# Optimization experiments

Measured on AMD Instinct MI355X. Metric: run time of the kernel, lower is better.

The kernel has to match this reference:

```python
import jax, jax.numpy as jnp
import numpy as np
import math

D_MODEL = 1024
NUM_HEADS = 16
BATCH = 2
SEQ = 2048

def setup_inputs() -> dict:
    key = jax.random.key(0)
    ks = jax.random.split(key, 9)
    s = 1.0 / math.sqrt(D_MODEL)
    inp = {
        "X": jax.random.normal(ks[0], (BATCH, SEQ, D_MODEL), dtype=jnp.float32),
        "Wq": jax.random.uniform(ks[1], (D_MODEL, D_MODEL), jnp.float32, -s, s),
        "bq": jax.random.uniform(ks[2], (D_MODEL,), jnp.float32, -s, s),
        "Wk": jax.random.uniform(ks[3], (D_MODEL, D_MODEL), jnp.float32, -s, s),
        "bk": jax.random.uniform(ks[4], (D_MODEL,), jnp.float32, -s, s),
        "Wv": jax.random.uniform(ks[5], (D_MODEL, D_MODEL), jnp.float32, -s, s),
        "bv": jax.random.uniform(ks[6], (D_MODEL,), jnp.float32, -s, s),
        "Wo": jax.random.uniform(ks[7], (D_MODEL, D_MODEL), jnp.float32, -s, s),
        "bo": jax.random.uniform(ks[8], (D_MODEL,), jnp.float32, -s, s),
    }
    return inp

def reference(X, Wq, bq, Wk, bk, Wv, bv, Wo, bo):
    B, S, D = X.shape
    H = NUM_HEADS
    dk = D // H
    # QKV projections (Linear: x @ W.T + b; here W stored as [in, out] so x @ W + b)
    q = X @ Wq + bq
    k = X @ Wk + bk
    v = X @ Wv + bv
    # split heads -> [B, H, S, dk]
    q = q.reshape(B, S, H, dk).transpose(0, 2, 1, 3)
    k = k.reshape(B, S, H, dk).transpose(0, 2, 1, 3)
    v = v.reshape(B, S, H, dk).transpose(0, 2, 1, 3)
    scores = jnp.einsum("bhqd,bhkd->bhqk", q, k) / math.sqrt(dk)
    weights = jax.nn.softmax(scores, axis=-1)
    attn = jnp.einsum("bhqk,bhkd->bhqd", weights, v)
    concat = attn.transpose(0, 2, 1, 3).reshape(B, S, D)
    return concat @ Wo + bo
```

## Files before the change

### kernel.cpp

```cpp
#include <hip/hip_runtime.h>
#include <stdint.h>

#define D_MODEL 1024
#define NH      16
#define DKH     64
#define BATCH   2
#define SEQ     2048
#define M_TOK   (BATCH*SEQ)

typedef __attribute__((ext_vector_type(8))) short bf16x8;
typedef __attribute__((ext_vector_type(4))) float f32x4;

__device__ __forceinline__ uint16_t f2b(float f) {
  uint32_t u = __builtin_bit_cast(uint32_t, f);
  return (uint16_t)((u + 0x7FFFu + ((u >> 16) & 1u)) >> 16);
}

__device__ __forceinline__ void gl2lds16(const uint16_t* g, uint16_t* l) {
  __builtin_amdgcn_global_load_lds(
      (const __attribute__((address_space(1))) void*)g,
      (__attribute__((address_space(3))) void*)l, 16, 0, 0);
}

__global__ __launch_bounds__(256) void prep(
    const float* __restrict__ X, uint16_t* __restrict__ Xb,
    const float* __restrict__ W0, const float* __restrict__ W1,
    const float* __restrict__ W2, const float* __restrict__ W3,
    uint16_t* __restrict__ T0, uint16_t* __restrict__ T1,
    uint16_t* __restrict__ T2, uint16_t* __restrict__ T3) {
  const int bid = blockIdx.x;
  if (bid < 2048) {
    int i = (bid * 256 + threadIdx.x) * 8;
    float4 a = *(const float4*)(X + i);
    float4 b = *(const float4*)(X + i + 4);
    uint16_t tmp[8] = {f2b(a.x), f2b(a.y), f2b(a.z), f2b(a.w),
                       f2b(b.x), f2b(b.y), f2b(b.z), f2b(b.w)};
    *(uint4*)(Xb + i) = *(const uint4*)tmp;
  } else {
    __shared__ float tile[32][33];
    int r = bid - 2048;
    int z = r >> 10, tt = r & 1023;
    const float* W = (z == 0) ? W0 : (z == 1) ? W1 : (z == 2) ? W2 : W3;
    uint16_t*    T = (z == 0) ? T0 : (z == 1) ? T1 : (z == 2) ? T2 : T3;
    int k0 = (tt & 31) * 32, n0 = (tt >> 5) * 32;
    int t = threadIdx.x;
    int rr = t >> 3, c4 = (t & 7) * 4;
    float4 v = *(const float4*)(W + (size_t)(k0 + rr) * D_MODEL + n0 + c4);
    tile[rr][c4] = v.x; tile[rr][c4 + 1] = v.y;
    tile[rr][c4 + 2] = v.z; tile[rr][c4 + 3] = v.w;
    __syncthreads();
    uint16_t o[4] = {f2b(tile[c4][rr]), f2b(tile[c4 + 1][rr]),
                     f2b(tile[c4 + 2][rr]), f2b(tile[c4 + 3][rr])};
    *(uint2*)(T + (size_t)(n0 + rr) * D_MODEL + k0 + c4) = *(const uint2*)o;
  }
}

template <bool SWAP>
__device__ __forceinline__ void gemm_core(const uint16_t* __restrict__ A,
                                          const uint16_t* __restrict__ BT,
                                          uint16_t* As, uint16_t* Bs,
                                          int m0, int n0, int kBeg, int kEnd,
                                          f32x4 (&acc)[4][4]) {
  const int t    = threadIdx.x;
  const int lane = t & 63;
  const int qi   = lane & 15, g = lane >> 4;
  const int wm   = (t >> 7) & 1;
  const int wn   = (t >> 6) & 1;
  const int srow = t >> 2;
  const int sc   = (t & 3) ^ ((t >> 3) & 3);
  const int wbase = t & 192;
  const int rch  = (g ^ ((qi >> 1) & 3)) * 8;

  const uint16_t* Ag = A  + (size_t)(m0 + srow) * D_MODEL + sc * 8;
  const uint16_t* Bg = BT + (size_t)(n0 + srow) * D_MODEL + sc * 8;

#pragma unroll
  for (int j = 0; j < 2; j++) {
    gl2lds16(Ag + (size_t)j * 64 * D_MODEL + kBeg, As + (j * 256 + wbase) * 8);
    gl2lds16(Bg + (size_t)j * 64 * D_MODEL + kBeg, Bs + (j * 256 + wbase) * 8);
  }

  int cur = 0;
  for (int k0 = kBeg; k0 < kEnd; k0 += 32) {
    __syncthreads();
    int kn = k0 + 32;
    if (kn < kEnd) {
      int nb = (cur ^ 1) * 4096;
#pragma unroll
      for (int j = 0; j < 2; j++) {
        gl2lds16(Ag + (size_t)j * 64 * D_MODEL + kn, As + nb + (j * 256 + wbase) * 8);
        gl2lds16(Bg + (size_t)j * 64 * D_MODEL + kn, Bs + nb + (j * 256 + wbase) * 8);
      }
    }
    const uint16_t* Ab = As + cur * 4096;
    const uint16_t* Bb = Bs + cur * 4096;
    bf16x8 af[4], bf[4];
#pragma unroll
    for (int i = 0; i < 4; i++) {
      af[i] = *(const bf16x8*)(Ab + (wm * 64 + i * 16 + qi) * 32 + rch);
      bf[i] = *(const bf16x8*)(Bb + (wn * 64 + i * 16 + qi) * 32 + rch);
    }
#pragma unroll
    for (int i = 0; i < 4; i++)
#pragma unroll
      for (int j = 0; j < 4; j++)
        acc[i][j] = SWAP
          ? __builtin_amdgcn_mfma_f32_16x16x32_bf16(bf[j], af[i], acc[i][j], 0, 0, 0)
          : __builtin_amdgcn_mfma_f32_16x16x32_bf16(af[i], bf[j], acc[i][j], 0, 0, 0);
    cur ^= 1;
  }
}

__global__ __launch_bounds__(256) void qkv_gemm(
    const uint16_t* __restrict__ Xb,
    const uint16_t* __restrict__ WqT, const uint16_t* __restrict__ WkT,
    const uint16_t* __restrict__ WvT,
    const float* __restrict__ bq, const float* __restrict__ bk,
    const float* __restrict__ bv,
    uint16_t* __restrict__ Qo, uint16_t* __restrict__ Ko, uint16_t* __restrict__ Vt) {
  __shared__ __align__(16) uint16_t smem[17408];
  uint16_t* As = smem;
  uint16_t* Bs = smem + 8192;
  uint16_t* T  = smem;
  const int z = blockIdx.z;
  const uint16_t* BT  = (z == 0) ? WqT : (z == 1) ? WkT : WvT;
  const float*   bias = (z == 0) ? bq  : (z == 1) ? bk  : bv;
  const int m0 = blockIdx.y * 128, n0 = blockIdx.x * 128;
  const int lane = threadIdx.x & 63, qi = lane & 15, g = lane >> 4;
  const int wm = (threadIdx.x >> 7) & 1, wn = (threadIdx.x >> 6) & 1;
  const float l2e = 1.4426950408889634f * 0.125f;

  const f32x4 ZERO = {0.f, 0.f, 0.f, 0.f};
  f32x4 acc[4][4];
#pragma unroll
  for (int i = 0; i < 4; i++)
#pragma unroll
    for (int j = 0; j < 4; j++) acc[i][j] = ZERO;

  if (z == 2) {
    gemm_core<false>(Xb, BT, As, Bs, m0, n0, 0, D_MODEL, acc);
    __syncthreads();
#pragma unroll
    for (int i = 0; i < 4; i++) {
      int tok = wm * 64 + i * 16 + g * 4;
#pragma unroll
      for (int j = 0; j < 4; j++) {
        int ch = wn * 64 + j * 16 + qi;
        float bb = bias[n0 + ch];
        uint32_t lo = (uint32_t)f2b(acc[i][j][0] + bb) | ((uint32_t)f2b(acc[i][j][1] + bb) << 16);
        uint32_t hi = (uint32_t)f2b(acc[i][j][2] + bb) | ((uint32_t)f2b(acc[i][j][3] + bb) << 16);
        uint2 pk = {lo, hi};
        *(uint2*)(T + ch * 136 + tok) = pk;
      }
    }
    __syncthreads();
    {
      int ch = threadIdx.x >> 1, sh = threadIdx.x & 1;
      const uint16_t* src = T + ch * 136 + sh * 64;
      int bidx = m0 >> 11;
      uint16_t* dst = Vt + ((size_t)(bidx * D_MODEL + n0 + ch)) * SEQ + (m0 & 2047) + sh * 64;
#pragma unroll
      for (int u = 0; u < 8; u++)
        *(uint4*)(dst + u * 8) = *(const uint4*)(src + u * 8);
    }
  } else {
    gemm_core<true>(Xb, BT, As, Bs, m0, n0, 0, D_MODEL, acc);
    uint16_t* O = z ? Ko : Qo;
    const float osc = (z == 0) ? l2e : 1.0f;
#pragma unroll
    for (int i = 0; i < 4; i++) {
      size_t tok = m0 + wm * 64 + i * 16 + qi;
#pragma unroll
      for (int j = 0; j < 4; j++) {
        int ch = n0 + wn * 64 + j * 16 + g * 4;
        float4 bb = *(const float4*)(bias + ch);
        uint32_t lo = (uint32_t)f2b((acc[i][j][0] + bb.x) * osc) |
                      ((uint32_t)f2b((acc[i][j][1] + bb.y) * osc) << 16);
        uint32_t hi = (uint32_t)f2b((acc[i][j][2] + bb.z) * osc) |
                      ((uint32_t)f2b((acc[i][j][3] + bb.w) * osc) << 16);
        uint2 pk = {lo, hi};
        *(uint2*)(O + tok * D_MODEL + ch) = pk;
      }
    }
  }
}

__global__ __launch_bounds__(256) void oproj_gemm(
    const uint16_t* __restrict__ Ab, const uint16_t* __restrict__ WoT,
    const float* __restrict__ bo, float* __restrict__ out) {
  __shared__ __align__(16) uint16_t As[8192];
  __shared__ __align__(16) uint16_t Bs[4096];
  const int t = threadIdx.x;
  const int lane = t & 63, qi = lane & 15, g = lane >> 4;
  const int wm = (t >> 7) & 1;
  const int wn = (t >> 6) & 1;
  const int srow = t >> 2;
  const int sc = (t & 3) ^ ((t >> 3) & 3);
  const int wbase = t & 192;
  const int rch = (g ^ ((qi >> 1) & 3)) * 8;
  const int m0 = blockIdx.y * 128, n0 = blockIdx.x * 64;

  const uint16_t* Ag = Ab  + (size_t)(m0 + srow) * D_MODEL + sc * 8;
  const uint16_t* Bg = WoT + (size_t)(n0 + srow) * D_MODEL + sc * 8;

  const f32x4 ZERO = {0.f, 0.f, 0.f, 0.f};
  f32x4 acc[4][2];
#pragma unroll
  for (int i = 0; i < 4; i++)
#pragma unroll
    for (int j = 0; j < 2; j++) acc[i][j] = ZERO;

  gl2lds16(Ag, As + wbase * 8);
  gl2lds16(Ag + (size_t)64 * D_MODEL, As + (256 + wbase) * 8);
  gl2lds16(Bg, Bs + wbase * 8);

  int cur = 0;
  for (int k0 = 0; k0 < D_MODEL; k0 += 32) {
    __syncthreads();
    int kn = k0 + 32;
    if (kn < D_MODEL) {
      int nbA = (cur ^ 1) * 4096, nbB = (cur ^ 1) * 2048;
      gl2lds16(Ag + kn, As + nbA + wbase * 8);
      gl2lds16(Ag + (size_t)64 * D_MODEL + kn, As + nbA + (256 + wbase) * 8);
      gl2lds16(Bg + kn, Bs + nbB + wbase * 8);
    }
    const uint16_t* Abuf = As + cur * 4096;
    const uint16_t* Bbuf = Bs + cur * 2048;
    bf16x8 af[4], bf[2];
#pragma unroll
    for (int i = 0; i < 4; i++)
      af[i] = *(const bf16x8*)(Abuf + (wm * 64 + i * 16 + qi) * 32 + rch);
#pragma unroll
    for (int j = 0; j < 2; j++)
      bf[j] = *(const bf16x8*)(Bbuf + (wn * 32 + j * 16 + qi) * 32 + rch);
#pragma unroll
    for (int i = 0; i < 4; i++)
#pragma unroll
      for (int j = 0; j < 2; j++)
        acc[i][j] = __builtin_amdgcn_mfma_f32_16x16x32_bf16(bf[j], af[i], acc[i][j], 0, 0, 0);
    cur ^= 1;
  }

#pragma unroll
  for (int i = 0; i < 4; i++) {
    size_t tok = m0 + wm * 64 + i * 16 + qi;
#pragma unroll
    for (int j = 0; j < 2; j++) {
      int ch = n0 + wn * 32 + j * 16 + g * 4;
      float4 bb = *(const float4*)(bo + ch);
      float4 o = {acc[i][j][0] + bb.x, acc[i][j][1] + bb.y,
                  acc[i][j][2] + bb.z, acc[i][j][3] + bb.w};
      *(float4*)(out + tok * D_MODEL + ch) = o;
    }
  }
}

__global__ __launch_bounds__(512, 2) void attn_fwd(
    const uint16_t* __restrict__ Q, const uint16_t* __restrict__ K,
    const uint16_t* __restrict__ Vt, uint16_t* __restrict__ O) {
  __shared__ __align__(16) uint16_t sm[36864];
  uint16_t* const Ps = sm + 20480;

  const int t = threadIdx.x, lane = t & 63, w = t >> 6;
  const int g = lane >> 4, qi = lane & 15;
  const int rch = (g ^ ((qi >> 1) & 3)) * 8;
  const int key = qi & 7;
  const int q0 = blockIdx.y * 256;
  const int bh = blockIdx.x, b = bh >> 4, h = bh & 15;
  const uint16_t* Qp = Q + (size_t)b * SEQ * D_MODEL + h * DKH;
  const uint16_t* Kp = K + (size_t)b * SEQ * D_MODEL + h * DKH;
  const uint16_t* Vp = Vt + (size_t)bh * DKH * SEQ;

  const int tt = t & 255, hs = t >> 8;
  const int srow = tt >> 2;
  const int sc = (tt & 3) ^ ((tt >> 3) & 3);
  const int wbase = tt & 192;

  bf16x8 qf[2][2];
#pragma unroll
  for (int i = 0; i < 2; i++) {
    const uint16_t* Qr = Qp + (size_t)(q0 + w * 32 + i * 16 + qi) * D_MODEL + g * 8;
    qf[0][i] = *(const bf16x8*)(Qr);
    qf[1][i] = *(const bf16x8*)(Qr + 32);
  }

  auto STAGE = [&](int tile, uint16_t* kb, uint16_t* vb) {
    gl2lds16(Kp + (size_t)(tile * 64 + srow) * D_MODEL + hs * 32 + sc * 8,
             kb + hs * 2048 + wbase * 8);
    gl2lds16(Vp + (size_t)srow * SEQ + tile * 64 + hs * 32 + sc * 8,
             vb + hs * 2048 + wbase * 8);
  };

  float lsum[2] = {0.f, 0.f};
  const f32x4 ZERO = {0.f, 0.f, 0.f, 0.f};
  f32x4 oaccT[4][2];
#pragma unroll
  for (int d = 0; d < 4; d++)
#pragma unroll
    for (int i = 0; i < 2; i++) oaccT[d][i] = ZERO;

  auto QK_SM = [&](const uint16_t* Kb) {
    f32x4 sacc[4][2];
#pragma unroll
    for (int j = 0; j < 4; j++)
#pragma unroll
      for (int i = 0; i < 2; i++) sacc[j][i] = ZERO;
#pragma unroll
    for (int ks = 0; ks < 2; ks++) {
      const uint16_t* Ksb = Kb + ks * 2048;
      bf16x8 kf[4];
#pragma unroll
      for (int j = 0; j < 4; j++)
        kf[j] = *(const bf16x8*)(Ksb + (j * 16 + qi) * 32 + rch);
      __builtin_amdgcn_s_setprio(1);
#pragma unroll
      for (int j = 0; j < 4; j++)
#pragma unroll
        for (int i = 0; i < 2; i++)
          sacc[j][i] = __builtin_amdgcn_mfma_f32_16x16x32_bf16(kf[j], qf[ks][i], sacc[j][i], 0, 0, 0);
      __builtin_amdgcn_s_setprio(0);
    }
#pragma unroll
    for (int i = 0; i < 2; i++) {
      uint16_t* Pr = Ps + (w * 32 + i * 16 + qi) * 64;
#pragma unroll
      for (int j = 0; j < 4; j++) {
        float p0 = __builtin_amdgcn_exp2f(sacc[j][i][0]);
        float p1 = __builtin_amdgcn_exp2f(sacc[j][i][1]);
        float p2 = __builtin_amdgcn_exp2f(sacc[j][i][2]);
        float p3 = __builtin_amdgcn_exp2f(sacc[j][i][3]);
        lsum[i] += (p0 + p1) + (p2 + p3);
        uint2 pk = {__builtin_amdgcn_perm(__builtin_bit_cast(uint32_t, p1),
                                          __builtin_bit_cast(uint32_t, p0), 0x07060302u),
                    __builtin_amdgcn_perm(__builtin_bit_cast(uint32_t, p3),
                                          __builtin_bit_cast(uint32_t, p2), 0x07060302u)};
        *(uint2*)(Pr + (((j * 4 + g) ^ (2 * key)) << 2)) = pk;
      }
    }
  };

  auto PV = [&](const uint16_t* Vb) {
#pragma unroll
    for (int ks = 0; ks < 2; ks++) {
      const uint16_t* Vsb = Vb + ks * 2048;
      bf16x8 vf[4], pf[2];
#pragma unroll
      for (int d = 0; d < 4; d++)
        vf[d] = *(const bf16x8*)(Vsb + (d * 16 + qi) * 32 + rch);
#pragma unroll
      for (int i = 0; i < 2; i++)
        pf[i] = *(const bf16x8*)(Ps + (w * 32 + i * 16 + qi) * 64 +
                                 (((ks * 4 + g) ^ key) << 3));
      __builtin_amdgcn_s_setprio(1);
#pragma unroll
      for (int d = 0; d < 4; d++)
#pragma unroll
        for (int i = 0; i < 2; i++)
          oaccT[d][i] = __builtin_amdgcn_mfma_f32_16x16x32_bf16(vf[d], pf[i], oaccT[d][i], 0, 0, 0);
      __builtin_amdgcn_s_setprio(0);
    }
  };

  STAGE(0, sm, sm + 8192);
  STAGE(1, sm + 4096, sm + 8192 + 4096);
  __syncthreads();
  QK_SM(sm);
  __syncthreads();

  for (int kt = 1; kt < SEQ / 64; kt++) {
    if (kt + 1 < SEQ / 64)
      STAGE(kt + 1, sm + ((kt + 1) & 1) * 4096,
            sm + 8192 + ((kt + 1) % 3) * 4096);
    const uint16_t* Kb = sm + (kt & 1) * 4096;
    const uint16_t* Vb = sm + 8192 + ((kt - 1) % 3) * 4096;
    PV(Vb);
    QK_SM(Kb);
    if (kt + 1 < SEQ / 64) __syncthreads();
  }
  PV(sm + 8192 + ((SEQ / 64 - 1) % 3) * 4096);

#pragma unroll
  for (int i = 0; i < 2; i++) {
    lsum[i] += __shfl_xor(lsum[i], 16, 64);
    lsum[i] += __shfl_xor(lsum[i], 32, 64);
  }
  float rl[2] = {1.f / lsum[0], 1.f / lsum[1]};

#pragma unroll
  for (int i = 0; i < 2; i++) {
    size_t row = (size_t)b * SEQ + q0 + w * 32 + i * 16 + qi;
#pragma unroll
    for (int d = 0; d < 4; d++) {
      uint32_t lo = (uint32_t)f2b(oaccT[d][i][0] * rl[i]) |
                    ((uint32_t)f2b(oaccT[d][i][1] * rl[i]) << 16);
      uint32_t hi = (uint32_t)f2b(oaccT[d][i][2] * rl[i]) |
                    ((uint32_t)f2b(oaccT[d][i][3] * rl[i]) << 16);
      uint2 pk = {lo, hi};
      *(uint2*)(O + row * D_MODEL + h * DKH + d * 16 + g * 4) = pk;
    }
  }
}

extern "C" void kernel_launch(void* const* d_in, const int* in_sizes, int n_in,
                              void* d_out, int out_size, void* d_ws, size_t ws_size,
                              hipStream_t stream) {
  (void)in_sizes; (void)n_in; (void)out_size; (void)ws_size;
  const float* X  = (const float*)d_in[0];
  const float* Wq = (const float*)d_in[1];
  const float* bq = (const float*)d_in[2];
  const float* Wk = (const float*)d_in[3];
  const float* bk = (const float*)d_in[4];
  const float* Wv = (const float*)d_in[5];
  const float* bv = (const float*)d_in[6];
  const float* Wo = (const float*)d_in[7];
  const float* bo = (const float*)d_in[8];
  float* out = (float*)d_out;

  char* p = (char*)d_ws;
  uint16_t* Xb  = (uint16_t*)p; p += (size_t)M_TOK * D_MODEL * 2;
  uint16_t* WqT = (uint16_t*)p; p += (size_t)D_MODEL * D_MODEL * 2;
  uint16_t* WkT = (uint16_t*)p; p += (size_t)D_MODEL * D_MODEL * 2;
  uint16_t* WvT = (uint16_t*)p; p += (size_t)D_MODEL * D_MODEL * 2;
  uint16_t* WoT = (uint16_t*)p; p += (size_t)D_MODEL * D_MODEL * 2;
  uint16_t* Qw  = (uint16_t*)p; p += (size_t)M_TOK * D_MODEL * 2;
  uint16_t* Kw  = (uint16_t*)p; p += (size_t)M_TOK * D_MODEL * 2;
  uint16_t* Vt  = (uint16_t*)p; p += (size_t)M_TOK * D_MODEL * 2;
  uint16_t* Ob  = (uint16_t*)p; p += (size_t)M_TOK * D_MODEL * 2;

  prep<<<6144, 256, 0, stream>>>(X, Xb, Wq, Wk, Wv, Wo, WqT, WkT, WvT, WoT);
  qkv_gemm<<<dim3(8, 32, 3), 256, 0, stream>>>(Xb, WqT, WkT, WvT, bq, bk, bv, Qw, Kw, Vt);
  attn_fwd<<<dim3(BATCH * NH, SEQ / 256), 512, 0, stream>>>(Qw, Kw, Vt, Ob);
  oproj_gemm<<<dim3(16, 32), 256, 0, stream>>>(Ob, WoT, bo, out);
}
```

Before: 191.3 us.

## Load K/V fragments directly from global memory in attention, drop LDS staging

The attention kernel no longer stages K and V tiles into shared memory with async global-to-LDS copies and double/triple buffering. Each wave now reads its K and V MFMA fragments straight from global memory into registers every key tile. Only the P tile stays in LDS, and the block shrinks to 256 threads with 128 queries, doubling the grid. This removes block-wide barriers and LDS traffic, but each wave redundantly fetches K/V through cache and loses the software prefetch, so load latency is exposed unless occupancy hides it.

```diff
diff --git a/kernel.cpp b/kernel.cpp
--- a/kernel.cpp
+++ b/kernel.cpp
@@ -255,27 +255,20 @@
   }
 }
 
-__global__ __launch_bounds__(512, 2) void attn_fwd(
+__global__ __launch_bounds__(256, 2) void attn_fwd(
     const uint16_t* __restrict__ Q, const uint16_t* __restrict__ K,
     const uint16_t* __restrict__ Vt, uint16_t* __restrict__ O) {
-  __shared__ __align__(16) uint16_t sm[36864];
-  uint16_t* const Ps = sm + 20480;
+  __shared__ __align__(16) uint16_t Ps[8192];
 
   const int t = threadIdx.x, lane = t & 63, w = t >> 6;
   const int g = lane >> 4, qi = lane & 15;
-  const int rch = (g ^ ((qi >> 1) & 3)) * 8;
   const int key = qi & 7;
-  const int q0 = blockIdx.y * 256;
+  const int q0 = blockIdx.y * 128;
   const int bh = blockIdx.x, b = bh >> 4, h = bh & 15;
   const uint16_t* Qp = Q + (size_t)b * SEQ * D_MODEL + h * DKH;
   const uint16_t* Kp = K + (size_t)b * SEQ * D_MODEL + h * DKH;
   const uint16_t* Vp = Vt + (size_t)bh * DKH * SEQ;
 
-  const int tt = t & 255, hs = t >> 8;
-  const int srow = tt >> 2;
-  const int sc = (tt & 3) ^ ((tt >> 3) & 3);
-  const int wbase = tt & 192;
-
   bf16x8 qf[2][2];
 #pragma unroll
   for (int i = 0; i < 2; i++) {
@@ -284,13 +277,6 @@
     qf[1][i] = *(const bf16x8*)(Qr + 32);
   }
 
-  auto STAGE = [&](int tile, uint16_t* kb, uint16_t* vb) {
-    gl2lds16(Kp + (size_t)(tile * 64 + srow) * D_MODEL + hs * 32 + sc * 8,
-             kb + hs * 2048 + wbase * 8);
-    gl2lds16(Vp + (size_t)srow * SEQ + tile * 64 + hs * 32 + sc * 8,
-             vb + hs * 2048 + wbase * 8);
-  };
-
   float lsum[2] = {0.f, 0.f};
   const f32x4 ZERO = {0.f, 0.f, 0.f, 0.f};
   f32x4 oaccT[4][2];
@@ -299,7 +285,15 @@
 #pragma unroll
     for (int i = 0; i < 2; i++) oaccT[d][i] = ZERO;
 
-  auto QK_SM = [&](const uint16_t* Kb) {
+  for (int kt = 0; kt < SEQ / 64; kt++) {
+    bf16x8 kf[2][4];
+#pragma unroll
+    for (int j = 0; j < 4; j++) {
+      const uint16_t* Kr = Kp + (size_t)(kt * 64 + j * 16 + qi) * D_MODEL + g * 8;
+      kf[0][j] = *(const bf16x8*)(Kr);
+      kf[1][j] = *(const bf16x8*)(Kr + 32);
+    }
+
     f32x4 sacc[4][2];
 #pragma unroll
     for (int j = 0; j < 4; j++)
@@ -307,19 +301,23 @@
       for (int i = 0; i < 2; i++) sacc[j][i] = ZERO;
 #pragma unroll
     for (int ks = 0; ks < 2; ks++) {
-      const uint16_t* Ksb = Kb + ks * 2048;
-      bf16x8 kf[4];
+      __builtin_amdgcn_s_setprio(1);
 #pragma unroll
       for (int j = 0; j < 4; j++)
-        kf[j] = *(const bf16x8*)(Ksb + (j * 16 + qi) * 32 + rch);
-      __builtin_amdgcn_s_setprio(1);
-#pragma unroll
-      for (int j = 0; j < 4; j++)
 #pragma unroll
         for (int i = 0; i < 2; i++)
-          sacc[j][i] = __builtin_amdgcn_mfma_f32_16x16x32_bf16(kf[j], qf[ks][i], sacc[j][i], 0, 0, 0);
+          sacc[j][i] = __builtin_amdgcn_mfma_f32_16x16x32_bf16(kf[ks][j], qf[ks][i], sacc[j][i], 0, 0, 0);
       __builtin_amdgcn_s_setprio(0);
     }
+
+    bf16x8 vf[2][4];
+#pragma unroll
+    for (int d = 0; d < 4; d++) {
+      const uint16_t* Vr = Vp + (size_t)(d * 16 + qi) * SEQ + kt * 64 + g * 8;
+      vf[0][d] = *(const bf16x8*)(Vr);
+      vf[1][d] = *(const bf16x8*)(Vr + 32);
+    }
+
 #pragma unroll
     for (int i = 0; i < 2; i++) {
       uint16_t* Pr = Ps + (w * 32 + i * 16 + qi) * 64;
@@ -337,16 +335,10 @@
         *(uint2*)(Pr + (((j * 4 + g) ^ (2 * key)) << 2)) = pk;
       }
     }
-  };
-
-  auto PV = [&](const uint16_t* Vb) {
+
 #pragma unroll
     for (int ks = 0; ks < 2; ks++) {
-      const uint16_t* Vsb = Vb + ks * 2048;
-      bf16x8 vf[4], pf[2];
-#pragma unroll
-      for (int d = 0; d < 4; d++)
-        vf[d] = *(const bf16x8*)(Vsb + (d * 16 + qi) * 32 + rch);
+      bf16x8 pf[2];
 #pragma unroll
       for (int i = 0; i < 2; i++)
         pf[i] = *(const bf16x8*)(Ps + (w * 32 + i * 16 + qi) * 64 +
@@ -356,28 +348,10 @@
       for (int d = 0; d < 4; d++)
 #pragma unroll
         for (int i = 0; i < 2; i++)
-          oaccT[d][i] = __builtin_amdgcn_mfma_f32_16x16x32_bf16(vf[d], pf[i], oaccT[d][i], 0, 0, 0);
+          oaccT[d][i] = __builtin_amdgcn_mfma_f32_16x16x32_bf16(vf[ks][d], pf[i], oaccT[d][i], 0, 0, 0);
       __builtin_amdgcn_s_setprio(0);
     }
-  };
-
-  STAGE(0, sm, sm + 8192);
-  STAGE(1, sm + 4096, sm + 8192 + 4096);
-  __syncthreads();
-  QK_SM(sm);
-  __syncthreads();
-
-  for (int kt = 1; kt < SEQ / 64; kt++) {
-    if (kt + 1 < SEQ / 64)
-      STAGE(kt + 1, sm + ((kt + 1) & 1) * 4096,
-            sm + 8192 + ((kt + 1) % 3) * 4096);
-    const uint16_t* Kb = sm + (kt & 1) * 4096;
-    const uint16_t* Vb = sm + 8192 + ((kt - 1) % 3) * 4096;
-    PV(Vb);
-    QK_SM(Kb);
-    if (kt + 1 < SEQ / 64) __syncthreads();
-  }
-  PV(sm + 8192 + ((SEQ / 64 - 1) % 3) * 4096);
+  }
 
 #pragma unroll
   for (int i = 0; i < 2; i++) {
@@ -429,6 +403,6 @@
 
   prep<<<6144, 256, 0, stream>>>(X, Xb, Wq, Wk, Wv, Wo, WqT, WkT, WvT, WoT);
   qkv_gemm<<<dim3(8, 32, 3), 256, 0, stream>>>(Xb, WqT, WkT, WvT, bq, bk, bv, Qw, Kw, Vt);
-  attn_fwd<<<dim3(BATCH * NH, SEQ / 256), 512, 0, stream>>>(Qw, Kw, Vt, Ob);
+  attn_fwd<<<dim3(BATCH * NH, SEQ / 128), 256, 0, stream>>>(Qw, Kw, Vt, Ob);
   oproj_gemm<<<dim3(16, 32), 256, 0, stream>>>(Ob, WoT, bo, out);
 }
```

New measurement: 264.9 us. 38.5% more time.
